# Kernel tuning notes

Measured on AMD Instinct MI355X. Metric: run time of the kernel, lower is better.

## Reference

```python
import math
import jax, jax.numpy as jnp
import numpy as np

D_MODEL = 1024
N_HEADS = 16
D_K = D_MODEL // N_HEADS
B, T = 2, 2048


def setup_inputs() -> dict:
    key = jax.random.key(0)
    kx, kq, kk, kv, ko = jax.random.split(key, 5)
    x = jax.random.normal(kx, (B, T, D_MODEL), dtype=jnp.float32)
    # causal mask, 1 = keep, 0 = masked (broadcast over batch & heads)
    mask = jnp.tril(jnp.ones((T, T), dtype=jnp.int32))[None, None, :, :]
    s = 1.0 / math.sqrt(D_MODEL)
    # nn.Linear stores weight as [out, in]; y = x @ W.T
    W_q = jax.random.normal(kq, (D_MODEL, D_MODEL), dtype=jnp.float32) * s
    W_k = jax.random.normal(kk, (D_MODEL, D_MODEL), dtype=jnp.float32) * s
    W_v = jax.random.normal(kv, (D_MODEL, D_MODEL), dtype=jnp.float32) * s
    W_o = jax.random.normal(ko, (D_MODEL, D_MODEL), dtype=jnp.float32) * s
    return {"x": x, "mask": mask, "W_q": W_q, "W_k": W_k, "W_v": W_v, "W_o": W_o}


def _split_heads(y):
    # [B,T,D] -> [B,H,T,d_k]
    b, t, _ = y.shape
    return y.reshape(b, t, N_HEADS, D_K).transpose(0, 2, 1, 3)


def reference(x, mask, W_q, W_k, W_v, W_o):
    Q = _split_heads(x @ W_q.T)
    K = _split_heads(x @ W_k.T)
    V = _split_heads(x @ W_v.T)
    scores = jnp.einsum("bhqd,bhkd->bhqk", Q, K) / math.sqrt(D_K)
    scores = jnp.where(mask == 0, -jnp.inf, scores)
    attn = jax.nn.softmax(scores, axis=-1)
    out = jnp.einsum("bhqk,bhkd->bhqd", attn, V)
    out = out.transpose(0, 2, 1, 3).reshape(x.shape[0], x.shape[1], D_MODEL)
    return out @ W_o.T
```

## Files before the change

### kernel.cpp

```cpp
#include <hip/hip_runtime.h>

typedef __attribute__((ext_vector_type(8))) short short8;
typedef __attribute__((ext_vector_type(4))) float f32x4;
typedef __attribute__((ext_vector_type(16))) float f32x16;
typedef __attribute__((ext_vector_type(4))) unsigned short u16x4;
typedef __attribute__((ext_vector_type(4))) unsigned int u32x4;

#define T_SEQ   2048
#define NHEADS  16
#define DHEAD   64
#define DMODEL  1024
#define NBATCH  2
#define MROWS   (NBATCH * T_SEQ)

__device__ __forceinline__ unsigned short f2bf(float f) {
    unsigned int u = __float_as_uint(f);
    u += 0x7fffu + ((u >> 16) & 1u);
    return (unsigned short)(u >> 16);
}

__device__ __forceinline__ unsigned int cvtpk(float lo, float hi) {
    unsigned int r;
    asm("v_cvt_pk_bf16_f32 %0, %1, %2" : "=v"(r) : "v"(lo), "v"(hi));
    return r;
}

__device__ __forceinline__ void pl32(int a, int b, int& r0, int& r1) {
    auto r = __builtin_amdgcn_permlane32_swap(a, b, false, false);
    r0 = r[0]; r1 = r[1];
}

__device__ __forceinline__ void gld_lds16(const unsigned short* g, unsigned short* l) {
    __builtin_amdgcn_global_load_lds(
        (const __attribute__((address_space(1))) void*)g,
        (__attribute__((address_space(3))) void*)l, 16, 0, 0);
}

#define N8X (MROWS * DMODEL / 8)
#define N8W (DMODEL * DMODEL / 8)
__global__ __launch_bounds__(256) void k_convert_all(const float* __restrict__ x,
                                                     const float* __restrict__ w0,
                                                     const float* __restrict__ w1,
                                                     const float* __restrict__ w2,
                                                     const float* __restrict__ w3,
                                                     unsigned short* __restrict__ xbf,
                                                     unsigned short* __restrict__ wbf) {
    int i = blockIdx.x * blockDim.x + threadIdx.x;
    const float* src;
    unsigned short* dst;
    if (i < N8X) {
        src = x + (size_t)i * 8;
        dst = xbf + (size_t)i * 8;
    } else {
        int j = i - N8X;
        int which = j >> 17;
        const float* w = (which == 0) ? w0 : (which == 1) ? w1 : (which == 2) ? w2 : w3;
        src = w + (size_t)(j & (N8W - 1)) * 8;
        dst = wbf + (size_t)j * 8;
    }
    const float4* p = (const float4*)src;
    float4 a = p[0], b = p[1];
    short8 r;
    r[0] = (short)f2bf(a.x); r[1] = (short)f2bf(a.y);
    r[2] = (short)f2bf(a.z); r[3] = (short)f2bf(a.w);
    r[4] = (short)f2bf(b.x); r[5] = (short)f2bf(b.y);
    r[6] = (short)f2bf(b.z); r[7] = (short)f2bf(b.w);
    *(short8*)dst = r;
}

template <int MODE>
__global__ __launch_bounds__(256) void k_gemm_st(const unsigned short* __restrict__ A,
                                                 const unsigned short* __restrict__ Wm,
                                                 float* __restrict__ outF,
                                                 unsigned short* __restrict__ outQ,
                                                 unsigned short* __restrict__ outK,
                                                 unsigned short* __restrict__ outV) {
    __shared__ __align__(16) unsigned short smA[2][128 * 32];
    __shared__ __align__(16) unsigned short smB[2][128 * 32];
    const int tid  = threadIdx.x;
    const int lane = tid & 63;
    const int w    = tid >> 6;
    const int lr   = lane & 15;
    const int lg   = lane >> 4;
    const int m0   = blockIdx.y * 128;
    const int n0   = blockIdx.x * 128;
    const int wm   = (w >> 1) * 64;
    const int wn   = (w & 1) * 64;

    const int srow = w * 32 + (lane >> 2);
    const int scol = (lane & 3) * 8;
    const unsigned short* gA0 = A  + (size_t)(m0 + srow) * DMODEL + scol;
    const unsigned short* gB0 = Wm + (size_t)(n0 + srow) * DMODEL + scol;
    const int lo = w * 1024;

    f32x4 acc[4][4];
#pragma unroll
    for (int i = 0; i < 4; i++)
#pragma unroll
        for (int j = 0; j < 4; j++) acc[i][j] = (f32x4){0.f, 0.f, 0.f, 0.f};

#define STAGE(K0, BUF) do {                                            \
        gld_lds16(gA0 + (K0),               smA[BUF] + lo);            \
        gld_lds16(gA0 + 16 * DMODEL + (K0), smA[BUF] + lo + 16 * 32);  \
        gld_lds16(gB0 + (K0),               smB[BUF] + lo);            \
        gld_lds16(gB0 + 16 * DMODEL + (K0), smB[BUF] + lo + 16 * 32);  \
    } while (0)

#define FRAG_READ(BUF)                                                           \
        short8 af[4], bfr[4];                                                    \
        {                                                                        \
            const unsigned short* sA = smA[BUF];                                 \
            const unsigned short* sB = smB[BUF];                                 \
            _Pragma("unroll")                                                    \
            for (int i = 0; i < 4; i++)                                          \
                af[i] = *(const short8*)&sA[(wm + 16 * i + lr) * 32 + lg * 8];   \
            _Pragma("unroll")                                                    \
            for (int j = 0; j < 4; j++)                                          \
                bfr[j] = *(const short8*)&sB[(wn + 16 * j + lr) * 32 + lg * 8];  \
        }

#define MFMA16()                                                                 \
        _Pragma("unroll")                                                        \
        for (int i = 0; i < 4; i++)                                              \
            _Pragma("unroll")                                                    \
            for (int j = 0; j < 4; j++)                                          \
                acc[i][j] = __builtin_amdgcn_mfma_f32_16x16x32_bf16(             \
                    af[i], bfr[j], acc[i][j], 0, 0, 0);

    STAGE(0, 0);
    STAGE(32, 1);

    for (int t = 0; t < 30; ++t) {
        asm volatile("s_waitcnt vmcnt(4)" ::: "memory");
        __builtin_amdgcn_s_barrier();
        FRAG_READ(t & 1)
        asm volatile("s_waitcnt lgkmcnt(0)" ::: "memory");
        __builtin_amdgcn_sched_barrier(0);
        __builtin_amdgcn_s_barrier();
        STAGE((t + 2) * 32, t & 1);
        MFMA16()
    }
    {
        asm volatile("s_waitcnt vmcnt(4)" ::: "memory");
        __builtin_amdgcn_s_barrier();
        FRAG_READ(0)
        MFMA16()
    }
    {
        asm volatile("s_waitcnt vmcnt(0)" ::: "memory");
        __builtin_amdgcn_s_barrier();
        FRAG_READ(1)
        MFMA16()
    }
#undef STAGE
#undef FRAG_READ
#undef MFMA16

    if (MODE == 0) {
#pragma unroll
        for (int i = 0; i < 4; i++)
#pragma unroll
            for (int j = 0; j < 4; j++) {
                int n = n0 + wn + 16 * j + lr;
#pragma unroll
                for (int r = 0; r < 4; r++) {
                    int mm = m0 + wm + 16 * i + lg * 4 + r;
                    outF[(size_t)mm * DMODEL + n] = acc[i][j][r];
                }
            }
    } else {
        const int which = n0 >> 10;
        const int nb = n0 & 1023;
        const float QS = 0.18033688f;
#pragma unroll
        for (int i = 0; i < 4; i++)
#pragma unroll
            for (int j = 0; j < 4; j++) {
                int nloc = nb + wn + 16 * j + lr;
                int h = nloc >> 6, d = nloc & 63;
                int mb = m0 + wm + 16 * i + lg * 4;
                int b = mb >> 11, t = mb & (T_SEQ - 1);
                size_t base = (size_t)(b * NHEADS + h) * T_SEQ * DHEAD;
                if (which == 2) {
                    int off = ((((t >> 6) * 2 + (d >> 5)) * 4 + ((t >> 4) & 3)) * 64
                               + ((t >> 3) & 1) * 32 + (d & 31)) * 8 + (t & 7);
                    u16x4 pk;
#pragma unroll
                    for (int r = 0; r < 4; r++) pk[r] = f2bf(acc[i][j][r]);
                    *(u16x4*)(outV + base + off) = pk;
                } else {
                    unsigned short* dst = (which == 0) ? outQ : outK;
                    const float sc = (which == 0) ? QS : 1.0f;
                    int off = (((t >> 5) * 4 + (d >> 4)) * 64 + (d & 8) * 4 + (t & 31)) * 8 + (d & 7);
#pragma unroll
                    for (int r = 0; r < 4; r++)
                        dst[base + off + r * 8] = f2bf(acc[i][j][r] * sc);
                }
            }
    }
}

__global__ __launch_bounds__(256) void k_attn(const unsigned short* __restrict__ Q,
                                              const unsigned short* __restrict__ K,
                                              const unsigned short* __restrict__ Vt,
                                              unsigned short* __restrict__ O) {
    __shared__ float Msm[3][64][33];
    const int tid  = threadIdx.x;
    const int lane = tid & 63;
    const int wv   = tid >> 6;
    const int l31  = lane & 31;
    const int hi   = lane >> 5;

    const int flat = blockIdx.x;
    const int xc   = flat & 7;
    const int rest = flat >> 3;
    const int hh   = rest >> 5;
    const int pr   = rest & 31;
    const int bh   = xc * 4 + hh;

    const size_t baseQK = (size_t)bh * T_SEQ * DHEAD;
    const unsigned short* Qb = Q  + baseQK;
    const unsigned short* Kb = K  + baseQK;
    const unsigned short* Vb = Vt + baseQK;

    for (int phase = 0; phase < 2; ++phase) {
        const int qt = phase ? pr : (63 - pr);
        const int q0 = qt * 32;
        const int ntiles = (qt >> 1) + 1;
        const int qlane = q0 + l31;

        short8 qf[4];
#pragma unroll
        for (int dt = 0; dt < 4; dt++)
            qf[dt] = *(const short8*)(Qb + ((size_t)(qt * 4 + dt) * 64 + lane) * 8);

        f32x16 oa0, oa1;
#pragma unroll
        for (int r = 0; r < 16; r++) { oa0[r] = 0.f; oa1[r] = 0.f; }
        float l = 0.f;

        for (int tix = wv; tix < ntiles; tix += 4) {
            f32x16 s0, s1;
#pragma unroll
            for (int r = 0; r < 16; r++) { s0[r] = 0.f; s1[r] = 0.f; }
            {
                short8 kf0[4], kf1[4];
#pragma unroll
                for (int kt = 0; kt < 4; kt++) {
                    kf0[kt] = *(const short8*)(Kb + ((size_t)((tix * 2)     * 4 + kt) * 64 + lane) * 8);
                    kf1[kt] = *(const short8*)(Kb + ((size_t)((tix * 2 + 1) * 4 + kt) * 64 + lane) * 8);
                }
                __builtin_amdgcn_s_setprio(1);
#pragma unroll
                for (int dt = 0; dt < 4; dt++)
                    s0 = __builtin_amdgcn_mfma_f32_32x32x16_bf16(kf0[dt], qf[dt], s0, 0, 0, 0);
#pragma unroll
                for (int dt = 0; dt < 4; dt++)
                    s1 = __builtin_amdgcn_mfma_f32_32x32x16_bf16(kf1[dt], qf[dt], s1, 0, 0, 0);
                __builtin_amdgcn_s_setprio(0);
            }

            short8 vf0[4], vf1[4];
#pragma unroll
            for (int kt = 0; kt < 4; kt++) {
                vf0[kt] = *(const short8*)(Vb + ((size_t)((tix * 2)     * 4 + kt) * 64 + lane) * 8);
                vf1[kt] = *(const short8*)(Vb + ((size_t)((tix * 2 + 1) * 4 + kt) * 64 + lane) * 8);
            }

            if (tix == ntiles - 1) {
                const int thr = qlane - tix * 64;
#pragma unroll
                for (int r = 0; r < 16; r++) {
                    const int koff = (r & 3) + 8 * (r >> 2) + 4 * hi;
                    if (koff > thr)      s0[r] = -1e30f;
                    if (koff + 32 > thr) s1[r] = -1e30f;
                }
            }

#pragma unroll
            for (int r = 0; r < 16; r++) {
                s0[r] = __builtin_amdgcn_exp2f(s0[r]);
                s1[r] = __builtin_amdgcn_exp2f(s1[r]);
            }
            float u8[8];
#pragma unroll
            for (int i = 0; i < 8; i++)
                u8[i] = (s0[i] + s0[i + 8]) + (s1[i] + s1[i + 8]);
            float u4a = u8[0] + u8[4], u4b = u8[1] + u8[5];
            float u4c = u8[2] + u8[6], u4d = u8[3] + u8[7];
            float sum = (u4a + u4b) + (u4c + u4d);
            {
                int r0, r1;
                pl32(__float_as_int(sum), __float_as_int(sum), r0, r1);
                sum = __int_as_float(r0) + __int_as_float(r1);
            }
            l += sum;

            unsigned int ow0[8], ow1[8];
#pragma unroll
            for (int q_ = 0; q_ < 8; q_++) {
                ow0[q_] = cvtpk(s0[2 * q_], s0[2 * q_ + 1]);
                ow1[q_] = cvtpk(s1[2 * q_], s1[2 * q_ + 1]);
            }

            __builtin_amdgcn_s_setprio(1);
#define PV_STEP(KT, OW, J) do {                                                  \
        int ra0, ra1, rb0, rb1;                                                  \
        pl32((int)OW[J],     (int)OW[J + 2], ra0, ra1);                          \
        pl32((int)OW[J + 1], (int)OW[J + 3], rb0, rb1);                          \
        u32x4 wvv;                                                               \
        wvv[0] = (unsigned)ra0; wvv[1] = (unsigned)rb0;                          \
        wvv[2] = (unsigned)ra1; wvv[3] = (unsigned)rb1;                          \
        short8 pf = __builtin_bit_cast(short8, wvv);                             \
        oa0 = __builtin_amdgcn_mfma_f32_32x32x16_bf16(vf0[KT], pf, oa0, 0, 0, 0);\
        oa1 = __builtin_amdgcn_mfma_f32_32x32x16_bf16(vf1[KT], pf, oa1, 0, 0, 0);\
    } while (0)

            PV_STEP(0, ow0, 0);
            PV_STEP(1, ow0, 4);
            PV_STEP(2, ow1, 0);
            PV_STEP(3, ow1, 4);
#undef PV_STEP
            __builtin_amdgcn_s_setprio(0);
        }

        const int merger = phase;
        if (phase == 1) __syncthreads();
        if (wv != merger) {
            const int slot = wv - (wv > merger ? 1 : 0);
#pragma unroll
            for (int r = 0; r < 16; r++) {
                Msm[slot][lane][r]      = oa0[r];
                Msm[slot][lane][16 + r] = oa1[r];
            }
            Msm[slot][lane][32] = l;
        }
        __syncthreads();
        if (wv == merger) {
            float lt = l;
#pragma unroll
            for (int s = 0; s < 3; s++) lt += Msm[s][lane][32];
            const float inv = 1.0f / lt;
            const int b = bh >> 4, h = bh & 15;
            unsigned short* orow = O + ((size_t)(b * T_SEQ + qlane)) * DMODEL + h * DHEAD;
#pragma unroll
            for (int rg = 0; rg < 4; rg++) {
                u16x4 pk0, pk1;
#pragma unroll
                for (int jj = 0; jj < 4; jj++) {
                    const int idx = 4 * rg + jj;
                    float v0 = oa0[idx];
                    float v1 = oa1[idx];
#pragma unroll
                    for (int s = 0; s < 3; s++) {
                        v0 += Msm[s][lane][idx];
                        v1 += Msm[s][lane][16 + idx];
                    }
                    pk0[jj] = f2bf(v0 * inv);
                    pk1[jj] = f2bf(v1 * inv);
                }
                *(u16x4*)(orow + 4 * hi + 8 * rg) = pk0;
                *(u16x4*)(orow + 32 + 4 * hi + 8 * rg) = pk1;
            }
        }
    }
}

extern "C" void kernel_launch(void* const* d_in, const int* in_sizes, int n_in,
                              void* d_out, int out_size, void* d_ws, size_t ws_size,
                              hipStream_t stream) {
    const float* x  = (const float*)d_in[0];
    const float* Wq = (const float*)d_in[2];
    const float* Wk = (const float*)d_in[3];
    const float* Wv = (const float*)d_in[4];
    const float* Wo = (const float*)d_in[5];

    unsigned short* wsu = (unsigned short*)d_ws;
    const size_t WELE = (size_t)DMODEL * DMODEL;
    unsigned short* Wo_bf = wsu + 3 * WELE;
    unsigned short* x_bf  = wsu + 4 * WELE;
    unsigned short* Qp    = wsu + 8 * WELE;
    unsigned short* Kp    = wsu + 12 * WELE;
    unsigned short* Vp    = wsu + 16 * WELE;
    if (ws_size < 20 * WELE * sizeof(unsigned short)) return;

    const int nAll = N8X + 4 * N8W;
    k_convert_all<<<dim3(nAll / 256), 256, 0, stream>>>(x, Wq, Wk, Wv, Wo, x_bf, wsu);

    k_gemm_st<1><<<dim3(3 * DMODEL / 128, MROWS / 128), 256, 0, stream>>>(
        x_bf, wsu, nullptr, Qp, Kp, Vp);

    k_attn<<<dim3(1024), 256, 0, stream>>>(Qp, Kp, Vp, x_bf);

    k_gemm_st<0><<<dim3(DMODEL / 128, MROWS / 128), 256, 0, stream>>>(
        x_bf, Wo_bf, (float*)d_out, nullptr, nullptr, nullptr);
}
```

Measured before the change: 102.7 us.

## Add dedicated 64x128-tile output projection GEMM with double-buffered LDS pipeline

Replaces the generic templated GEMM for the output projection with a specialized kernel using 64x128 tiles, which doubles the block count (512 vs 256) to better fill the GPU's compute units. It double-buffers K-slices of 32 in LDS via direct global-to-LDS loads and overlaps the next stage's loads with MFMA work. Smaller tiles mean less reuse per block and more global traffic for the weight matrix.

```diff
diff --git a/kernel.cpp b/kernel.cpp
--- a/kernel.cpp
+++ b/kernel.cpp
@@ -200,6 +200,104 @@
     }
 }
 
+__global__ __launch_bounds__(256) void k_gemm_o(const unsigned short* __restrict__ A,
+                                                const unsigned short* __restrict__ Wm,
+                                                float* __restrict__ outF) {
+    __shared__ __align__(16) unsigned short smA[2][64 * 32];
+    __shared__ __align__(16) unsigned short smB[2][128 * 32];
+    const int tid  = threadIdx.x;
+    const int lane = tid & 63;
+    const int w    = tid >> 6;
+    const int lr   = lane & 15;
+    const int lg   = lane >> 4;
+    const int m0   = blockIdx.y * 64;
+    const int n0   = blockIdx.x * 128;
+    const int wm   = (w >> 1) * 32;
+    const int wn   = (w & 1) * 64;
+
+    const int srA  = w * 16 + (lane >> 2);
+    const int srB  = w * 32 + (lane >> 2);
+    const int scol = (lane & 3) * 8;
+    const unsigned short* gA0 = A  + (size_t)(m0 + srA) * DMODEL + scol;
+    const unsigned short* gB0 = Wm + (size_t)(n0 + srB) * DMODEL + scol;
+    const int loA = w * 512;
+    const int loB = w * 1024;
+
+    f32x4 acc[2][4];
+#pragma unroll
+    for (int i = 0; i < 2; i++)
+#pragma unroll
+        for (int j = 0; j < 4; j++) acc[i][j] = (f32x4){0.f, 0.f, 0.f, 0.f};
+
+#define STAGE(K0, BUF) do {                                            \
+        gld_lds16(gA0 + (K0),               smA[BUF] + loA);           \
+        gld_lds16(gB0 + (K0),               smB[BUF] + loB);           \
+        gld_lds16(gB0 + 16 * DMODEL + (K0), smB[BUF] + loB + 16 * 32); \
+    } while (0)
+
+#define FRAG_READ(BUF)                                                           \
+        short8 af[2], bfr[4];                                                    \
+        {                                                                        \
+            const unsigned short* sA = smA[BUF];                                 \
+            const unsigned short* sB = smB[BUF];                                 \
+            _Pragma("unroll")                                                    \
+            for (int i = 0; i < 2; i++)                                          \
+                af[i] = *(const short8*)&sA[(wm + 16 * i + lr) * 32 + lg * 8];   \
+            _Pragma("unroll")                                                    \
+            for (int j = 0; j < 4; j++)                                          \
+                bfr[j] = *(const short8*)&sB[(wn + 16 * j + lr) * 32 + lg * 8];  \
+        }
+
+#define MFMA8()                                                                  \
+        _Pragma("unroll")                                                        \
+        for (int i = 0; i < 2; i++)                                              \
+            _Pragma("unroll")                                                    \
+            for (int j = 0; j < 4; j++)                                          \
+                acc[i][j] = __builtin_amdgcn_mfma_f32_16x16x32_bf16(             \
+                    af[i], bfr[j], acc[i][j], 0, 0, 0);
+
+    STAGE(0, 0);
+    STAGE(32, 1);
+
+    for (int t = 0; t < 30; ++t) {
+        asm volatile("s_waitcnt vmcnt(3)" ::: "memory");
+        __builtin_amdgcn_s_barrier();
+        FRAG_READ(t & 1)
+        asm volatile("s_waitcnt lgkmcnt(0)" ::: "memory");
+        __builtin_amdgcn_sched_barrier(0);
+        __builtin_amdgcn_s_barrier();
+        STAGE((t + 2) * 32, t & 1);
+        MFMA8()
+    }
+    {
+        asm volatile("s_waitcnt vmcnt(3)" ::: "memory");
+        __builtin_amdgcn_s_barrier();
+        FRAG_READ(0)
+        MFMA8()
+    }
+    {
+        asm volatile("s_waitcnt vmcnt(0)" ::: "memory");
+        __builtin_amdgcn_s_barrier();
+        FRAG_READ(1)
+        MFMA8()
+    }
+#undef STAGE
+#undef FRAG_READ
+#undef MFMA8
+
+#pragma unroll
+    for (int i = 0; i < 2; i++)
+#pragma unroll
+        for (int j = 0; j < 4; j++) {
+            int n = n0 + wn + 16 * j + lr;
+#pragma unroll
+            for (int r = 0; r < 4; r++) {
+                int mm = m0 + wm + 16 * i + lg * 4 + r;
+                outF[(size_t)mm * DMODEL + n] = acc[i][j][r];
+            }
+        }
+}
+
 __global__ __launch_bounds__(256) void k_attn(const unsigned short* __restrict__ Q,
                                               const unsigned short* __restrict__ K,
                                               const unsigned short* __restrict__ Vt,
@@ -392,6 +490,6 @@
 
     k_attn<<<dim3(1024), 256, 0, stream>>>(Qp, Kp, Vp, x_bf);
 
-    k_gemm_st<0><<<dim3(DMODEL / 128, MROWS / 128), 256, 0, stream>>>(
-        x_bf, Wo_bf, (float*)d_out, nullptr, nullptr, nullptr);
-}
+    k_gemm_o<<<dim3(DMODEL / 128, MROWS / 64), 256, 0, stream>>>(
+        x_bf, Wo_bf, (float*)d_out);
+}
```

Result: no change. 101.7 us (-1.0%).
